# Kernel tuning notes

Hardware: AMD Instinct MI355X
Metric: run time of the kernel (lower is better)

The kernel has to match this reference:

```python
import jax, jax.numpy as jnp
import numpy as np

N_NODES = 50000
N_EDGES = 1600000
N_FEATURES = 1433
HIDDEN = 256
N_CLASSES = 7


def setup_inputs() -> dict:
    key = jax.random.key(0)
    ks = jax.random.split(key, 5)
    x = jax.random.normal(ks[0], (N_NODES, N_FEATURES), dtype=jnp.float32)
    edge_index = jax.random.randint(ks[1], (2, N_EDGES), 0, N_NODES, dtype=jnp.int64)
    # Glorot-style init like PyG's Linear inside GCNConv
    W1 = jax.random.normal(ks[2], (N_FEATURES, HIDDEN), dtype=jnp.float32) * (1.0 / np.sqrt(N_FEATURES))
    b1 = jnp.zeros((HIDDEN,), dtype=jnp.float32)
    W2 = jax.random.normal(ks[3], (HIDDEN, N_CLASSES), dtype=jnp.float32) * (1.0 / np.sqrt(HIDDEN))
    b2 = jnp.zeros((N_CLASSES,), dtype=jnp.float32)
    return {"x": x, "edge_index": edge_index, "W1": W1, "b1": b1, "W2": W2, "b2": b2}


def _gcn_conv(x, W, b, src, dst, n_nodes):
    """PyG GCNConv: add self-loops, symmetric deg^{-1/2} norm, linear, scatter-add, +bias."""
    h = x @ W  # [N, out]
    loop = jnp.arange(n_nodes, dtype=src.dtype)
    src2 = jnp.concatenate([src, loop])
    dst2 = jnp.concatenate([dst, loop])
    ones = jnp.ones(src2.shape[0], dtype=h.dtype)
    deg = jax.ops.segment_sum(ones, dst2, num_segments=n_nodes)
    dinv = jnp.where(deg > 0, jax.lax.rsqrt(deg), 0.0)
    norm = dinv[src2] * dinv[dst2]  # [E+N]
    msg = h[src2] * norm[:, None]   # gather + scale
    out = jax.ops.segment_sum(msg, dst2, num_segments=n_nodes)
    return out + b


def reference(x, edge_index, W1, b1, W2, b2):
    src, dst = edge_index[0], edge_index[1]
    h = _gcn_conv(x, W1, b1, src, dst, N_NODES)
    h = jax.nn.relu(h)
    # dropout p=0.5 is identity in eval mode (training=False)
    out = _gcn_conv(h, W2, b2, src, dst, N_NODES)
    return out
```

## Files before the change

kernel.cpp:

```cpp
#include <hip/hip_runtime.h>
#include <hip/hip_bf16.h>


#define N_NODES_   50000
#define NB_ROWS_   50048
#define N_EDGES_   1600000
#define N_FEAT_    1433
#define K_PAD_     1440
#define HIDDEN_    256
#define N_CLASSES_ 7
#define NPART_     ((N_NODES_ + 255) / 256)

typedef __attribute__((ext_vector_type(8))) short short8;
typedef __attribute__((ext_vector_type(8))) unsigned short ushort8;
typedef __attribute__((ext_vector_type(4))) float f32x4;
typedef unsigned int u32;
typedef unsigned short u16;

__device__ __forceinline__ u16 f2bf(float f) {
    __hip_bfloat16 h = __float2bfloat16(f);
    return *(u16*)&h;
}
__device__ __forceinline__ float bf2f(u16 u) {
    return __uint_as_float((u32)u << 16);
}
__device__ __forceinline__ void global_to_lds16(const void* g, void* l) {
    __builtin_amdgcn_global_load_lds(
        (const __attribute__((address_space(1))) u32*)g,
        (__attribute__((address_space(3))) u32*)l, 16, 0, 0);
}

__global__ void deg_kernel(const int* __restrict__ dst, int* __restrict__ deg) {
    int i = blockIdx.x * blockDim.x + threadIdx.x;
    if (i < N_EDGES_) atomicAdd(&deg[dst[i]], 1);
}

__global__ void dinv_kernel(const int* __restrict__ deg, float* __restrict__ dinv) {
    int i = blockIdx.x * blockDim.x + threadIdx.x;
    if (i < N_NODES_) dinv[i] = rsqrtf((float)(deg[i] + 1));
}

__global__ __launch_bounds__(256) void scan1_kernel(const int* __restrict__ deg,
                                                    int* __restrict__ partial) {
    __shared__ int ws[4];
    int t = threadIdx.x, b = blockIdx.x;
    int idx = b * 256 + t;
    int v = (idx < N_NODES_) ? deg[idx] : 0;
    #pragma unroll
    for (int off = 32; off > 0; off >>= 1) v += __shfl_down(v, off, 64);
    if ((t & 63) == 0) ws[t >> 6] = v;
    __syncthreads();
    if (t == 0) partial[b] = ws[0] + ws[1] + ws[2] + ws[3];
}

__global__ __launch_bounds__(256) void scan2_kernel(int* __restrict__ partial,
                                                    int* __restrict__ blk_off) {
    __shared__ int sh[256];
    int t = threadIdx.x;
    int v = (t < NPART_) ? partial[t] : 0;
    sh[t] = v;
    __syncthreads();
    #pragma unroll
    for (int off = 1; off < 256; off <<= 1) {
        int a = (t >= off) ? sh[t - off] : 0;
        __syncthreads();
        sh[t] += a;
        __syncthreads();
    }
    if (t < NPART_) blk_off[t] = sh[t] - v;
}

__global__ __launch_bounds__(256) void scan3_kernel(const int* __restrict__ deg,
                                                    const int* __restrict__ blk_off,
                                                    int* __restrict__ row_ptr,
                                                    int* __restrict__ cursor) {
    __shared__ int sh[256];
    int t = threadIdx.x, b = blockIdx.x;
    int idx = b * 256 + t;
    int v = (idx < N_NODES_) ? deg[idx] : 0;
    sh[t] = v;
    __syncthreads();
    #pragma unroll
    for (int off = 1; off < 256; off <<= 1) {
        int a = (t >= off) ? sh[t - off] : 0;
        __syncthreads();
        sh[t] += a;
        __syncthreads();
    }
    if (idx < N_NODES_) {
        int rp = blk_off[b] + sh[t] - v;
        row_ptr[idx] = rp;
        cursor[idx]  = rp;
    }
    if (idx == 0) row_ptr[N_NODES_] = N_EDGES_;
}

__global__ void csr_scatter_kernel(const int* __restrict__ src, const int* __restrict__ dst,
                                   int* __restrict__ cursor, int* __restrict__ csr_src) {
    int i = blockIdx.x * blockDim.x + threadIdx.x;
    if (i >= N_EDGES_) return;
    int d = dst[i];
    int pos = atomicAdd(&cursor[d], 1);
    csr_src[pos] = src[i];
}

__global__ void w1t_kernel(const float* __restrict__ W1, u16* __restrict__ W1T) {
    int gid = blockIdx.x * blockDim.x + threadIdx.x;
    if (gid >= HIDDEN_ * K_PAD_) return;
    int k = gid % K_PAD_, n = gid / K_PAD_;
    float v = (k < N_FEAT_) ? W1[(long)k * HIDDEN_ + n] : 0.f;
    W1T[(long)n * K_PAD_ + k] = f2bf(v);
}

__global__ __launch_bounds__(256) void gemm1_fused(const float* __restrict__ X,
                                                   const u16* __restrict__ BT,
                                                   const float* __restrict__ dinv,
                                                   u16* __restrict__ C) {
    __shared__ u16 As[64 * 32];
    __shared__ u16 Bs[256 * 32];

    const int tid  = threadIdx.x;
    const int lane = tid & 63;
    const int wv   = tid >> 6;
    const int row0 = blockIdx.x * 64;
    const int wc0  = wv * 64;

    f32x4 acc[4][4] = {};

    const int srow = lane >> 2;
    const int skk  = (lane & 3) * 8;
    const int ar = tid >> 5;
    const int ak = tid & 31;
    const int kmax = N_FEAT_ - 1;

    for (int k0 = 0; k0 < K_PAD_; k0 += 32) {
        #pragma unroll
        for (int j = 0; j < 4; j++) {
            int rbase = j * 64 + wv * 16;
            const u16* g = BT + (long)(rbase + srow) * K_PAD_ + k0 + skk;
            global_to_lds16(g, &Bs[rbase * 32]);
        }
        int kcl = min(k0 + ak, kmax);
        float av[8];
        #pragma unroll
        for (int j = 0; j < 8; j++) {
            int rcl = min(row0 + ar + j * 8, N_NODES_ - 1);
            av[j] = X[(long)rcl * N_FEAT_ + kcl];
        }
        #pragma unroll
        for (int j = 0; j < 8; j++)
            As[(ar + j * 8) * 32 + ak] = f2bf(av[j]);
        __syncthreads();

        const int fm = lane & 15;
        const int fq = (lane >> 4) * 8;
        short8 af[4], bf[4];
        #pragma unroll
        for (int mi = 0; mi < 4; mi++)
            af[mi] = *(const short8*)&As[(mi * 16 + fm) * 32 + fq];
        #pragma unroll
        for (int ni = 0; ni < 4; ni++)
            bf[ni] = *(const short8*)&Bs[(wc0 + ni * 16 + fm) * 32 + fq];
        #pragma unroll
        for (int mi = 0; mi < 4; mi++)
            #pragma unroll
            for (int ni = 0; ni < 4; ni++)
                acc[mi][ni] = __builtin_amdgcn_mfma_f32_16x16x32_bf16(af[mi], bf[ni], acc[mi][ni], 0, 0, 0);
        __syncthreads();
    }

    const int fm = lane & 15;
    const int q4 = (lane >> 4) * 4;
    #pragma unroll
    for (int mi = 0; mi < 4; mi++) {
        #pragma unroll
        for (int r = 0; r < 4; r++) {
            int gm = row0 + mi * 16 + q4 + r;
            if (gm < N_NODES_) {
                float sc = dinv[gm];
                #pragma unroll
                for (int ni = 0; ni < 4; ni++) {
                    int gn = wc0 + ni * 16 + fm;
                    C[(long)gm * HIDDEN_ + gn] = f2bf(acc[mi][ni][r] * sc);
                }
            }
        }
    }
}

__global__ __launch_bounds__(256) void agg_gemm2_kernel(const u16* __restrict__ h1s,
                                                        const int* __restrict__ row_ptr,
                                                        const int* __restrict__ csr_src,
                                                        const float* __restrict__ dinv,
                                                        const float* __restrict__ b1,
                                                        const float* __restrict__ W2,
                                                        float* __restrict__ h2s) {
    __shared__ float w2s[HIDDEN_ * N_CLASSES_];
    __shared__ float b1s[HIDDEN_];
    int tid = threadIdx.x;
    for (int i = tid; i < HIDDEN_ * N_CLASSES_; i += 256) w2s[i] = W2[i];
    for (int i = tid; i < HIDDEN_; i += 256) b1s[i] = b1[i];
    __syncthreads();

    int wave = tid >> 6;
    int lane = tid & 63;
    int node = blockIdx.x * 4 + wave;
    if (node >= N_NODES_) return;

    int e0 = row_ptr[node], e1 = row_ptr[node + 1];
    float ax = 0.f, ay = 0.f, az = 0.f, aw = 0.f;

    int sL = (e0 + lane < e1) ? csr_src[e0 + lane] : N_NODES_;
    for (int base = e0; base < e1; base += 64) {
        int sCur = sL;
        int nb = base + 64;
        if (nb < e1) sL = (nb + lane < e1) ? csr_src[nb + lane] : N_NODES_;
        int cnt8 = (min(64, e1 - base) + 7) & ~7;
        for (int j = 0; j < cnt8; j += 8) {
            #pragma unroll
            for (int t = 0; t < 8; t++) {
                int s = __shfl(sCur, j + t, 64);
                ushort4 u = ((const ushort4*)(h1s + (long)s * HIDDEN_))[lane];
                ax += bf2f(u.x);
                ay += bf2f(u.y);
                az += bf2f(u.z);
                aw += bf2f(u.w);
            }
        }
    }
    float nd = dinv[node];
    ushort4 su = ((const ushort4*)(h1s + (long)node * HIDDEN_))[lane];
    float xv[4];
    xv[0] = fmaxf((ax + bf2f(su.x)) * nd + b1s[lane * 4 + 0], 0.f);
    xv[1] = fmaxf((ay + bf2f(su.y)) * nd + b1s[lane * 4 + 1], 0.f);
    xv[2] = fmaxf((az + bf2f(su.z)) * nd + b1s[lane * 4 + 2], 0.f);
    xv[3] = fmaxf((aw + bf2f(su.w)) * nd + b1s[lane * 4 + 3], 0.f);

    float p[N_CLASSES_];
    #pragma unroll
    for (int c = 0; c < N_CLASSES_; c++) {
        float a = 0.f;
        #pragma unroll
        for (int i = 0; i < 4; i++)
            a += xv[i] * w2s[(lane * 4 + i) * N_CLASSES_ + c];
        p[c] = a;
    }
    #pragma unroll
    for (int off = 32; off > 0; off >>= 1)
        #pragma unroll
        for (int c = 0; c < N_CLASSES_; c++)
            p[c] += __shfl_down(p[c], off, 64);
    if (lane == 0) {
        #pragma unroll
        for (int c = 0; c < N_CLASSES_; c++)
            h2s[(long)node * 8 + c] = p[c] * nd;
    }
}

__global__ void out_kernel(const float* __restrict__ h2s,
                           const int* __restrict__ row_ptr,
                           const int* __restrict__ csr_src,
                           const float* __restrict__ dinv,
                           const float* __restrict__ b2,
                           float* __restrict__ out) {
    long gid = (long)blockIdx.x * blockDim.x + threadIdx.x;
    int node = (int)(gid >> 3);
    int c = (int)(gid & 7);
    if (node >= N_NODES_ || c >= N_CLASSES_) return;
    int e0 = row_ptr[node], e1 = row_ptr[node + 1];
    float acc = 0.f;
    for (int e = e0; e < e1; e += 4) {
        int s0 = csr_src[e];
        int s1 = (e + 1 < e1) ? csr_src[e + 1] : N_NODES_;
        int s2 = (e + 2 < e1) ? csr_src[e + 2] : N_NODES_;
        int s3 = (e + 3 < e1) ? csr_src[e + 3] : N_NODES_;
        float v0 = h2s[(long)s0 * 8 + c];
        float v1 = h2s[(long)s1 * 8 + c];
        float v2 = h2s[(long)s2 * 8 + c];
        float v3 = h2s[(long)s3 * 8 + c];
        acc += (v0 + v1) + (v2 + v3);
    }
    float nd = dinv[node];
    out[(long)node * N_CLASSES_ + c] =
        (acc + h2s[(long)node * 8 + c]) * nd + b2[c];
}

extern "C" void kernel_launch(void* const* d_in, const int* in_sizes, int n_in,
                              void* d_out, int out_size, void* d_ws, size_t ws_size,
                              hipStream_t stream) {
    const float* x   = (const float*)d_in[0];
    const int*   ei  = (const int*)d_in[1];
    const int*   src = ei;
    const int*   dst = ei + N_EDGES_;
    const float* W1  = (const float*)d_in[2];
    const float* b1  = (const float*)d_in[3];
    const float* W2  = (const float*)d_in[4];
    const float* b2  = (const float*)d_in[5];
    float* out = (float*)d_out;

    char* ws = (char*)d_ws;
    size_t off = 0;
    auto alloc = [&](size_t bytes) { void* p = ws + off; off = (off + bytes + 255) & ~(size_t)255; return p; };
    u16*   h1s     = (u16*)alloc((size_t)(N_NODES_ + 1) * HIDDEN_ * 2);
    u16*   w1t     = (u16*)alloc((size_t)HIDDEN_ * K_PAD_ * 2);
    float* h2s     = (float*)alloc((size_t)(N_NODES_ + 1) * 8 * 4);
    int*   deg     = (int*)alloc((size_t)N_NODES_ * 4);
    float* dinv    = (float*)alloc((size_t)N_NODES_ * 4);
    int*   row_ptr = (int*)alloc((size_t)(N_NODES_ + 1) * 4);
    int*   cursor  = (int*)alloc((size_t)N_NODES_ * 4);
    int*   csr_src = (int*)alloc((size_t)N_EDGES_ * 4);
    int*   partial = (int*)alloc((size_t)NPART_ * 4);
    int*   blk_off = (int*)alloc((size_t)NPART_ * 4);

    hipMemsetAsync(deg, 0, (size_t)N_NODES_ * 4, stream);
    hipMemsetAsync(h1s + (size_t)N_NODES_ * HIDDEN_, 0, HIDDEN_ * 2, stream);
    hipMemsetAsync(h2s + (size_t)N_NODES_ * 8, 0, 8 * 4, stream);

    deg_kernel<<<(N_EDGES_ + 255) / 256, 256, 0, stream>>>(dst, deg);
    dinv_kernel<<<(N_NODES_ + 255) / 256, 256, 0, stream>>>(deg, dinv);
    scan1_kernel<<<NPART_, 256, 0, stream>>>(deg, partial);
    scan2_kernel<<<1, 256, 0, stream>>>(partial, blk_off);
    scan3_kernel<<<NPART_, 256, 0, stream>>>(deg, blk_off, row_ptr, cursor);
    csr_scatter_kernel<<<(N_EDGES_ + 255) / 256, 256, 0, stream>>>(src, dst, cursor, csr_src);

    w1t_kernel<<<(HIDDEN_ * K_PAD_ + 255) / 256, 256, 0, stream>>>(W1, w1t);

    gemm1_fused<<<NB_ROWS_ / 64, 256, 0, stream>>>(x, w1t, dinv, h1s);

    agg_gemm2_kernel<<<(N_NODES_ + 3) / 4, 256, 0, stream>>>(h1s, row_ptr, csr_src, dinv, b1, W2, h2s);

    long out_threads = (long)N_NODES_ * 8;
    out_kernel<<<(unsigned)((out_threads + 255) / 256), 256, 0, stream>>>(h2s, row_ptr, csr_src, dinv, b2, out);
}
```

Before: 811.5 us.

## Double-buffer gemm1 LDS tiles with XOR swizzle and halve row tile to 32

Rewrites the first GEMM main loop to double-buffer the A and B tiles in LDS. The next K-slice is prefetched from global memory while MFMAs run on the current one, and only one barrier is used per iteration. An XOR swizzle on LDS columns is added to avoid bank conflicts, and the block row tile is halved from 64 to 32 rows, which doubles the grid. The trade-off is that B is reloaded by twice as many blocks, raising global and L2 traffic for W1T, in exchange for more occupancy and latency hiding.

```diff
diff --git a/kernel.cpp b/kernel.cpp
--- a/kernel.cpp
+++ b/kernel.cpp
@@ -10,6 +10,7 @@
 #define HIDDEN_    256
 #define N_CLASSES_ 7
 #define NPART_     ((N_NODES_ + 255) / 256)
+#define NT_        (K_PAD_ / 32)
 
 typedef __attribute__((ext_vector_type(8))) short short8;
 typedef __attribute__((ext_vector_type(8))) unsigned short ushort8;
@@ -116,63 +117,111 @@
                                                    const u16* __restrict__ BT,
                                                    const float* __restrict__ dinv,
                                                    u16* __restrict__ C) {
-    __shared__ u16 As[64 * 32];
-    __shared__ u16 Bs[256 * 32];
+    __shared__ u16 As[2 * 32 * 32];
+    __shared__ u16 Bs[2 * 256 * 32];
 
     const int tid  = threadIdx.x;
     const int lane = tid & 63;
     const int wv   = tid >> 6;
-    const int row0 = blockIdx.x * 64;
-    const int wc0  = wv * 64;
-
-    f32x4 acc[4][4] = {};
-
-    const int srow = lane >> 2;
-    const int skk  = (lane & 3) * 8;
+    const int row0 = blockIdx.x * 32;
+
+    f32x4 acc[2][4] = {};
+
     const int ar = tid >> 5;
     const int ak = tid & 31;
-    const int kmax = N_FEAT_ - 1;
-
-    for (int k0 = 0; k0 < K_PAD_; k0 += 32) {
+    const int awc = (ak >> 3);
+    const int awo = (ak & 7);
+    const int srow = lane >> 2;
+    const int ch   = lane & 3;
+    const int fm = lane & 15;
+    const int q  = lane >> 4;
+
+    float av[4];
+
+    #pragma unroll
+    for (int j = 0; j < 4; j++) {
+        int rcl = min(row0 + ar + 8 * j, N_NODES_ - 1);
+        av[j] = X[(long)rcl * N_FEAT_ + ak];
+    }
+    #pragma unroll
+    for (int j = 0; j < 4; j++) {
+        int rb = j * 64 + wv * 16;
+        int r  = rb + srow;
+        int c  = ch ^ ((r >> 1) & 3);
+        global_to_lds16(BT + (long)r * K_PAD_ + 8 * c, &Bs[rb * 32]);
+    }
+    #pragma unroll
+    for (int j = 0; j < 4; j++) {
+        int r = ar + 8 * j;
+        As[r * 32 + ((awc ^ ((r >> 1) & 3)) << 3) + awo] = f2bf(av[j]);
+    }
+    __syncthreads();
+
+    int buf = 0;
+    for (int t = 0; t < NT_ - 1; ++t) {
+        const int k0n = (t + 1) * 32;
+        int kcl = min(k0n + ak, N_FEAT_ - 1);
         #pragma unroll
         for (int j = 0; j < 4; j++) {
-            int rbase = j * 64 + wv * 16;
-            const u16* g = BT + (long)(rbase + srow) * K_PAD_ + k0 + skk;
-            global_to_lds16(g, &Bs[rbase * 32]);
-        }
-        int kcl = min(k0 + ak, kmax);
-        float av[8];
-        #pragma unroll
-        for (int j = 0; j < 8; j++) {
-            int rcl = min(row0 + ar + j * 8, N_NODES_ - 1);
+            int rcl = min(row0 + ar + 8 * j, N_NODES_ - 1);
             av[j] = X[(long)rcl * N_FEAT_ + kcl];
         }
         #pragma unroll
-        for (int j = 0; j < 8; j++)
-            As[(ar + j * 8) * 32 + ak] = f2bf(av[j]);
-        __syncthreads();
-
-        const int fm = lane & 15;
-        const int fq = (lane >> 4) * 8;
-        short8 af[4], bf[4];
-        #pragma unroll
-        for (int mi = 0; mi < 4; mi++)
-            af[mi] = *(const short8*)&As[(mi * 16 + fm) * 32 + fq];
-        #pragma unroll
-        for (int ni = 0; ni < 4; ni++)
-            bf[ni] = *(const short8*)&Bs[(wc0 + ni * 16 + fm) * 32 + fq];
-        #pragma unroll
-        for (int mi = 0; mi < 4; mi++)
+        for (int j = 0; j < 4; j++) {
+            int rb = j * 64 + wv * 16;
+            int r  = rb + srow;
+            int c  = ch ^ ((r >> 1) & 3);
+            global_to_lds16(BT + (long)r * K_PAD_ + k0n + 8 * c,
+                            &Bs[(buf ^ 1) * 8192 + rb * 32]);
+        }
+        short8 af[2], bfr[4];
+        #pragma unroll
+        for (int mi = 0; mi < 2; mi++) {
+            int ra = mi * 16 + fm;
+            af[mi] = *(const short8*)&As[buf * 1024 + ra * 32 + ((q ^ ((ra >> 1) & 3)) << 3)];
+        }
+        #pragma unroll
+        for (int ni = 0; ni < 4; ni++) {
+            int rb2 = wv * 64 + ni * 16 + fm;
+            bfr[ni] = *(const short8*)&Bs[buf * 8192 + rb2 * 32 + ((q ^ ((rb2 >> 1) & 3)) << 3)];
+        }
+        #pragma unroll
+        for (int mi = 0; mi < 2; mi++)
             #pragma unroll
             for (int ni = 0; ni < 4; ni++)
-                acc[mi][ni] = __builtin_amdgcn_mfma_f32_16x16x32_bf16(af[mi], bf[ni], acc[mi][ni], 0, 0, 0);
-        __syncthreads();
-    }
-
-    const int fm = lane & 15;
+                acc[mi][ni] = __builtin_amdgcn_mfma_f32_16x16x32_bf16(af[mi], bfr[ni], acc[mi][ni], 0, 0, 0);
+        __builtin_amdgcn_sched_barrier(0);
+        #pragma unroll
+        for (int j = 0; j < 4; j++) {
+            int r = ar + 8 * j;
+            As[(buf ^ 1) * 1024 + r * 32 + ((awc ^ ((r >> 1) & 3)) << 3) + awo] = f2bf(av[j]);
+        }
+        __syncthreads();
+        buf ^= 1;
+    }
+
+    {
+        short8 af[2], bfr[4];
+        #pragma unroll
+        for (int mi = 0; mi < 2; mi++) {
+            int ra = mi * 16 + fm;
+            af[mi] = *(const short8*)&As[buf * 1024 + ra * 32 + ((q ^ ((ra >> 1) & 3)) << 3)];
+        }
+        #pragma unroll
+        for (int ni = 0; ni < 4; ni++) {
+            int rb2 = wv * 64 + ni * 16 + fm;
+            bfr[ni] = *(const short8*)&Bs[buf * 8192 + rb2 * 32 + ((q ^ ((rb2 >> 1) & 3)) << 3)];
+        }
+        #pragma unroll
+        for (int mi = 0; mi < 2; mi++)
+            #pragma unroll
+            for (int ni = 0; ni < 4; ni++)
+                acc[mi][ni] = __builtin_amdgcn_mfma_f32_16x16x32_bf16(af[mi], bfr[ni], acc[mi][ni], 0, 0, 0);
+    }
+
     const int q4 = (lane >> 4) * 4;
     #pragma unroll
-    for (int mi = 0; mi < 4; mi++) {
+    for (int mi = 0; mi < 2; mi++) {
         #pragma unroll
         for (int r = 0; r < 4; r++) {
             int gm = row0 + mi * 16 + q4 + r;
@@ -180,7 +229,7 @@
                 float sc = dinv[gm];
                 #pragma unroll
                 for (int ni = 0; ni < 4; ni++) {
-                    int gn = wc0 + ni * 16 + fm;
+                    int gn = wv * 64 + ni * 16 + fm;
                     C[(long)gm * HIDDEN_ + gn] = f2bf(acc[mi][ni][r] * sc);
                 }
             }
@@ -325,7 +374,7 @@
 
     w1t_kernel<<<(HIDDEN_ * K_PAD_ + 255) / 256, 256, 0, stream>>>(W1, w1t);
 
-    gemm1_fused<<<NB_ROWS_ / 64, 256, 0, stream>>>(x, w1t, dinv, h1s);
+    gemm1_fused<<<NB_ROWS_ / 32, 256, 0, stream>>>(x, w1t, dinv, h1s);
 
     agg_gemm2_kernel<<<(N_NODES_ + 3) / 4, 256, 0, stream>>>(h1s, row_ptr, csr_src, dinv, b1, W2, h2s);
 
```

After: 828.5 us. 2.1% more time.
